# Kernel optimization log

Hardware: AMD Instinct MI355X
Metric: run time of the kernel (lower is better)

## Reference

```python
import jax, jax.numpy as jnp
import numpy as np

N = 20000      # nodes
E = 320000     # directed edges (before self loops)
IN_DIM = 384
D = 256        # hidden_dim
H = 4          # heads
C = D // H     # per-head channels = 64
L = 3          # layers
NEG_SLOPE = 0.2
LN_EPS = 1e-5


def setup_inputs() -> dict:
    key = jax.random.key(0)
    ks = jax.random.split(key, 8)
    return {
        "x": jax.random.normal(ks[0], (N, IN_DIM), jnp.float32),
        "edge_index": jax.random.randint(ks[1], (2, E), 0, N),
        "w_in": jax.random.normal(ks[2], (IN_DIM, D), jnp.float32) * 0.05,
        "b_in": jnp.zeros((D,), jnp.float32),
        "wl": jax.random.normal(ks[3], (L, D, D), jnp.float32) * 0.05,
        "wr": jax.random.normal(ks[4], (L, D, D), jnp.float32) * 0.05,
        "att": jax.random.normal(ks[5], (L, H, C), jnp.float32) * 0.05,
        "bias": jnp.zeros((L, D), jnp.float32),
        "ln_g": jnp.ones((L, D), jnp.float32),
        "ln_b": jnp.zeros((L, D), jnp.float32),
    }


def _layernorm(h, g, b):
    mu = jnp.mean(h, axis=-1, keepdims=True)
    var = jnp.mean(jnp.square(h - mu), axis=-1, keepdims=True)
    return (h - mu) * jax.lax.rsqrt(var + LN_EPS) * g + b


def _gatv2(h, src, dst, Wl, Wr, a, b):
    # PyG GATv2Conv, concat=True, eval mode (no dropout), self-loops already in src/dst.
    xl = (h @ Wl).reshape(N, H, C)   # source transform (lin_l)
    xr = (h @ Wr).reshape(N, H, C)   # target transform (lin_r)
    x_j = xl[src]                    # [E', H, C] gathered source messages
    e = jnp.einsum('ehc,hc->eh', jax.nn.leaky_relu(x_j + xr[dst], NEG_SLOPE), a)
    # segment softmax over edges grouped by destination node
    m = jax.ops.segment_max(e, dst, num_segments=N)
    e = jnp.exp(e - m[dst])
    s = jax.ops.segment_sum(e, dst, num_segments=N)
    alpha = e / (s[dst] + 1e-16)     # [E', H]
    out = jax.ops.segment_sum(x_j * alpha[:, :, None], dst, num_segments=N)
    return out.reshape(N, D) + b


def reference(x, edge_index, w_in, b_in, wl, wr, att, bias, ln_g, ln_b):
    loops = jnp.arange(N, dtype=edge_index.dtype)
    src = jnp.concatenate([edge_index[0], loops])
    dst = jnp.concatenate([edge_index[1], loops])
    h = x @ w_in + b_in
    for l in range(L):
        h_new = _layernorm(_gatv2(h, src, dst, wl[l], wr[l], att[l], bias[l]),
                           ln_g[l], ln_b[l])
        h = h + h_new  # shapes always match since concat output == hidden_dim
    norm = jnp.linalg.norm(h, axis=-1, keepdims=True)
    return h / jnp.maximum(norm, 1e-12)
```

## Files before the change

### kernel.cpp

```cpp
#include <hip/hip_runtime.h>
#include <math.h>

#define N_NODES 20000
#define E_EDGES 320000
#define E_TOT   (E_EDGES + N_NODES)
#define IN_DIM  384
#define DIM     256
#define LAYERS  3
#define NEG_SLOPE 0.2f
#define LN_EPS 1e-5f

typedef unsigned short u16;
typedef unsigned int u32;
typedef __attribute__((ext_vector_type(8))) short short8;
typedef __attribute__((ext_vector_type(8))) __bf16 bf16x8;
typedef __attribute__((ext_vector_type(4))) float f32x4;

__device__ inline u16 f2bf(float f) {
    u32 u = __builtin_bit_cast(u32, f);
    return (u16)((u + 0x7fffu + ((u >> 16) & 1u)) >> 16);
}
__device__ inline float bf2f(u16 s) {
    u32 u = (u32)s << 16;
    return __builtin_bit_cast(float, u);
}

__device__ inline float2 f2add(float2 a, float2 b) { return make_float2(a.x + b.x, a.y + b.y); }
__device__ inline float2 f2mul(float2 a, float2 b) { return make_float2(a.x * b.x, a.y * b.y); }
__device__ inline float2 f2fma(float2 a, float2 b, float2 c) {
    return make_float2(fmaf(a.x, b.x, c.x), fmaf(a.y, b.y, c.y));
}
__device__ inline float2 f2max(float2 a, float2 b) {
    return make_float2(fmaxf(a.x, b.x), fmaxf(a.y, b.y));
}

__device__ inline f32x4 mfma_bf16(short8 a, short8 b, f32x4 c) {
    return __builtin_amdgcn_mfma_f32_16x16x32_bf16(
        __builtin_bit_cast(bf16x8, a), __builtin_bit_cast(bf16x8, b), c, 0, 0, 0);
}

__device__ inline void gl_lds16(const u16* g, u16* l) {
    __builtin_amdgcn_global_load_lds(
        (const __attribute__((address_space(1))) u32*)g,
        (__attribute__((address_space(3))) u32*)l, 16, 0, 0);
}

#define W_IN_ELEMS (IN_DIM * DIM)
#define W_LR_ELEMS (2 * DIM * DIM)
#define W_TOT (W_IN_ELEMS + LAYERS * W_LR_ELEMS)

#define N4X (N_NODES * IN_DIM / 4)
__global__ void prep_kernel(const int* __restrict__ ei, int* __restrict__ counts,
                            const float* __restrict__ x, u16* __restrict__ x_bf,
                            const float* __restrict__ w_in, const float* __restrict__ wl,
                            const float* __restrict__ wr, u16* __restrict__ w_out) {
    int tid = blockIdx.x * 256 + threadIdx.x;
    if (tid < E_TOT) {
        int d = (tid < E_EDGES) ? ei[E_EDGES + tid] : (tid - E_EDGES);
        atomicAdd(&counts[d], 1);
        return;
    }
    tid -= E_TOT;
    if (tid < N4X) {
        float4 v = reinterpret_cast<const float4*>(x)[tid];
        reinterpret_cast<ushort4*>(x_bf)[tid] =
            make_ushort4(f2bf(v.x), f2bf(v.y), f2bf(v.z), f2bf(v.w));
        return;
    }
    tid -= N4X;
    if (tid < W_TOT) {
        float v;
        if (tid < W_IN_ELEMS) {
            int n = tid / IN_DIM, k = tid % IN_DIM;
            v = w_in[k * DIM + n];
        } else {
            int j = tid - W_IN_ELEMS;
            int l = j / W_LR_ELEMS;
            int r = j % W_LR_ELEMS;
            int n = r >> 8, k = r & 255;
            const float* W = (n < DIM) ? wl : wr;
            v = W[l * DIM * DIM + k * DIM + (n & 255)];
        }
        w_out[tid] = f2bf(v);
    }
}

__global__ __launch_bounds__(1024) void scan_kernel(const int* __restrict__ counts,
                                                    int* __restrict__ row_ptr) {
    __shared__ int sums[1024];
    const int t = threadIdx.x;
    const int CH = (N_NODES + 1023) / 1024;
    int base = t * CH;
    int local = 0;
    for (int i = 0; i < CH; ++i) {
        int idx = base + i;
        if (idx < N_NODES) local += counts[idx];
    }
    sums[t] = local;
    __syncthreads();
    for (int off = 1; off < 1024; off <<= 1) {
        int v = (t >= off) ? sums[t - off] : 0;
        __syncthreads();
        sums[t] += v;
        __syncthreads();
    }
    int run = (t == 0) ? 0 : sums[t - 1];
    for (int i = 0; i < CH; ++i) {
        int idx = base + i;
        if (idx < N_NODES) { row_ptr[idx] = run; run += counts[idx]; }
    }
    if (t == 1023) row_ptr[N_NODES] = sums[1023];
}

__global__ void scatter_kernel(const int* __restrict__ ei, const int* __restrict__ row_ptr,
                               int* __restrict__ cursor, int* __restrict__ csr_src) {
    int e = blockIdx.x * 256 + threadIdx.x;
    if (e >= E_TOT) return;
    int s, d;
    if (e < E_EDGES) { s = ei[e]; d = ei[E_EDGES + e]; }
    else { s = e - E_EDGES; d = s; }
    int pos = row_ptr[d] + atomicAdd(&cursor[d], 1);
    csr_src[pos] = s;
}

#define BM 128
#define BN 128
#define BK 64
template <int K, bool BIAS, int NX, int NTOT>
__global__ __launch_bounds__(256) void gemm_mfma(
    const u16* __restrict__ A, const u16* __restrict__ B,
    const float* __restrict__ bias, u16* __restrict__ Cbf,
    int M, int ldc) {
    __shared__ u16 lds[2][2][BM * BK];
    const int tid = threadIdx.x;
    const int w = tid >> 6, lane = tid & 63;
    const int wm = w >> 1, wn = w & 1;

    int lin = blockIdx.y * NX + blockIdx.x;
    constexpr int q8 = NTOT >> 3, r8 = NTOT & 7;
    int k8 = lin & 7, j8 = lin >> 3;
    int bid2 = k8 * q8 + min(k8, r8) + j8;
    const int bm = (bid2 / NX) * BM, bn = (bid2 % NX) * BN;

    const int fr = lane & 15, q = lane >> 4;

    f32x4 acc[4][4] = {};

    const int s_row = tid >> 3, s_blk = tid & 7;
    constexpr int NT = K / BK;

#pragma unroll
    for (int i = 0; i < 4; ++i) {
        int row = i * 32 + s_row;
        int gcol = ((s_blk ^ (row & 7)) << 3);
        int base = (i * 256 + (tid & ~63)) << 3;
        int ra = min(bm + row, M - 1);
        gl_lds16(A + (size_t)ra * K + gcol, &lds[0][0][base]);
        gl_lds16(B + (size_t)(bn + row) * K + gcol, &lds[0][1][base]);
    }
    __syncthreads();

    for (int t = 0; t < NT; ++t) {
        const int p = t & 1;
        if (t + 1 < NT) {
            const int k0 = (t + 1) * BK;
#pragma unroll
            for (int i = 0; i < 4; ++i) {
                int row = i * 32 + s_row;
                int gcol = ((s_blk ^ (row & 7)) << 3);
                int base = (i * 256 + (tid & ~63)) << 3;
                int ra = min(bm + row, M - 1);
                gl_lds16(A + (size_t)ra * K + k0 + gcol, &lds[p ^ 1][0][base]);
                gl_lds16(B + (size_t)(bn + row) * K + k0 + gcol, &lds[p ^ 1][1][base]);
            }
        }
        short8 a_f[2][4], b_f[2][4];
#pragma unroll
        for (int kk = 0; kk < 2; ++kk) {
#pragma unroll
            for (int mi = 0; mi < 4; ++mi) {
                int row = wm * 64 + mi * 16 + fr;
                a_f[kk][mi] = *reinterpret_cast<const short8*>(
                    &lds[p][0][row * BK + ((((kk << 2) + q) ^ (row & 7)) << 3)]);
            }
#pragma unroll
            for (int ni = 0; ni < 4; ++ni) {
                int row = wn * 64 + ni * 16 + fr;
                b_f[kk][ni] = *reinterpret_cast<const short8*>(
                    &lds[p][1][row * BK + ((((kk << 2) + q) ^ (row & 7)) << 3)]);
            }
        }
#pragma unroll
        for (int kk = 0; kk < 2; ++kk)
#pragma unroll
            for (int mi = 0; mi < 4; ++mi)
#pragma unroll
                for (int ni = 0; ni < 4; ++ni)
                    acc[mi][ni] = mfma_bf16(a_f[kk][mi], b_f[kk][ni], acc[mi][ni]);
        __syncthreads();
    }

#pragma unroll
    for (int mi = 0; mi < 4; ++mi) {
#pragma unroll
        for (int r = 0; r < 4; ++r) {
            int row = bm + wm * 64 + mi * 16 + q * 4 + r;
            if (row >= M) continue;
#pragma unroll
            for (int ni = 0; ni < 4; ++ni) {
                int col = bn + wn * 64 + ni * 16 + fr;
                float v = acc[mi][ni][r];
                if (BIAS) v += bias[col];
                Cbf[(size_t)row * ldc + col] = f2bf(v);
            }
        }
    }
}

template <bool LAST>
__global__ __launch_bounds__(256) void gat_edge(const u16* __restrict__ xlr_bf,
                                                const int* __restrict__ row_ptr,
                                                const int* __restrict__ csr_src,
                                                const float* __restrict__ att,
                                                const float* __restrict__ bias,
                                                const float* __restrict__ ln_g,
                                                const float* __restrict__ ln_b,
                                                u16* __restrict__ h_bf,
                                                float* __restrict__ out) {
    const int wave = threadIdx.x >> 6;
    const int lane = threadIdx.x & 63;
    const int node = blockIdx.x * 4 + wave;
    if (node >= N_NODES) return;
    const int c4 = lane << 2;

    const float4 a4 = *reinterpret_cast<const float4*>(att + c4);
    const float2 a01 = make_float2(a4.x, a4.y), a23 = make_float2(a4.z, a4.w);
    const ushort4 uxr = *reinterpret_cast<const ushort4*>(xlr_bf + (size_t)node * 512 + 256 + c4);
    const float2 xr01 = make_float2(bf2f(uxr.x), bf2f(uxr.y));
    const float2 xr23 = make_float2(bf2f(uxr.z), bf2f(uxr.w));
    const float2 k02 = make_float2(NEG_SLOPE, NEG_SLOPE);

    float sA = 0.f, sB = 0.f;
    float2 aA01 = make_float2(0.f, 0.f), aA23 = aA01, aB01 = aA01, aB23 = aA01;

    const int e0 = row_ptr[node];
    const int d = row_ptr[node + 1] - e0;

    for (int base = 0; base < d; base += 64) {
        const int rem = min(d - base, 64);
        const int idx = base + lane;
        const int my_src = (idx < d) ? csr_src[e0 + idx] : node;
        for (int k = 0; k < rem; k += 4) {
            ushort4 uu[4];
#pragma unroll
            for (int j = 0; j < 4; ++j) {
                int s = __shfl(my_src, k + j);
                uu[j] = *reinterpret_cast<const ushort4*>(xlr_bf + (size_t)s * 512 + c4);
            }
#pragma unroll
            for (int j = 0; j < 4; ++j) {
                float2 v01 = make_float2(bf2f(uu[j].x), bf2f(uu[j].y));
                float2 v23 = make_float2(bf2f(uu[j].z), bf2f(uu[j].w));
                float2 t01 = f2add(v01, xr01), t23 = f2add(v23, xr23);
                float2 l01 = f2max(t01, f2mul(t01, k02));
                float2 l23 = f2max(t23, f2mul(t23, k02));
                float2 dd = f2fma(l01, a01, f2mul(l23, a23));
                float p = dd.x + dd.y;
                p += __shfl_xor(p, 1);
                p += __shfl_xor(p, 2);
                p += __shfl_xor(p, 4);
                p += __shfl_xor(p, 8);
                float pe = (k + j < rem) ? __expf(p) : 0.f;
                float2 pe2 = make_float2(pe, pe);
                if (j & 1) {
                    sB += pe;
                    aB01 = f2fma(pe2, v01, aB01);
                    aB23 = f2fma(pe2, v23, aB23);
                } else {
                    sA += pe;
                    aA01 = f2fma(pe2, v01, aA01);
                    aA23 = f2fma(pe2, v23, aA23);
                }
            }
        }
    }

    float s = sA + sB;
    float inv = 1.f / (s + 1e-16f);
    float2 inv2 = make_float2(inv, inv);
    float2 acc01 = f2add(aA01, aB01), acc23 = f2add(aA23, aB23);
    const float4 b4 = *reinterpret_cast<const float4*>(bias + c4);
    float2 o01 = f2fma(acc01, inv2, make_float2(b4.x, b4.y));
    float2 o23 = f2fma(acc23, inv2, make_float2(b4.z, b4.w));

    float lsum = o01.x + o01.y + o23.x + o23.y;
    float lsq = o01.x * o01.x + o01.y * o01.y + o23.x * o23.x + o23.y * o23.y;
#pragma unroll
    for (int off = 1; off < 64; off <<= 1) {
        lsum += __shfl_xor(lsum, off);
        lsq  += __shfl_xor(lsq, off);
    }
    float mu = lsum * (1.f / 256.f);
    float var = lsq * (1.f / 256.f) - mu * mu;
    float rstd = rsqrtf(var + LN_EPS);
    const float4 g4  = *reinterpret_cast<const float4*>(ln_g + c4);
    const float4 lb4 = *reinterpret_cast<const float4*>(ln_b + c4);
    float2 mu2 = make_float2(-mu, -mu), rstd2 = make_float2(rstd, rstd);

    const ushort4 uh = *reinterpret_cast<const ushort4*>(h_bf + (size_t)node * DIM + c4);
    float2 h01 = make_float2(bf2f(uh.x), bf2f(uh.y));
    float2 h23 = make_float2(bf2f(uh.z), bf2f(uh.w));
    float2 n01 = f2fma(f2mul(f2add(o01, mu2), rstd2), make_float2(g4.x, g4.y),
                       make_float2(lb4.x, lb4.y));
    float2 n23 = f2fma(f2mul(f2add(o23, mu2), rstd2), make_float2(g4.z, g4.w),
                       make_float2(lb4.z, lb4.w));
    h01 = f2add(h01, n01);
    h23 = f2add(h23, n23);

    if (LAST) {
        float nsq = h01.x * h01.x + h01.y * h01.y + h23.x * h23.x + h23.y * h23.y;
#pragma unroll
        for (int off = 1; off < 64; off <<= 1) nsq += __shfl_xor(nsq, off);
        float ninv = 1.f / fmaxf(sqrtf(nsq), 1e-12f);
        float4 o = make_float4(h01.x * ninv, h01.y * ninv, h23.x * ninv, h23.y * ninv);
        *reinterpret_cast<float4*>(out + (size_t)node * DIM + c4) = o;
    } else {
        *reinterpret_cast<ushort4*>(h_bf + (size_t)node * DIM + c4) =
            make_ushort4(f2bf(h01.x), f2bf(h01.y), f2bf(h23.x), f2bf(h23.y));
    }
}

extern "C" void kernel_launch(void* const* d_in, const int* in_sizes, int n_in,
                              void* d_out, int out_size, void* d_ws, size_t ws_size,
                              hipStream_t stream) {
    const float* x    = (const float*)d_in[0];
    const int*   ei   = (const int*)d_in[1];
    const float* w_in = (const float*)d_in[2];
    const float* b_in = (const float*)d_in[3];
    const float* wl   = (const float*)d_in[4];
    const float* wr   = (const float*)d_in[5];
    const float* att  = (const float*)d_in[6];
    const float* bias = (const float*)d_in[7];
    const float* ln_g = (const float*)d_in[8];
    const float* ln_b = (const float*)d_in[9];

    char* p = (char*)d_ws;
    u16*   h_bf   = (u16*)p;              p += (size_t)N_NODES * DIM * 2;
    u16*   xlr_bf = (u16*)p;              p += (size_t)N_NODES * 512 * 2;
    u16*   w_bf   = (u16*)p;              p += (size_t)W_TOT * 2;
    int* row_ptr  = (int*)p;              p += (N_NODES + 1) * 4;
    int* counts   = (int*)p;              p += N_NODES * 4;
    int* cursor   = (int*)p;              p += N_NODES * 4;
    int* csr_src  = (int*)p;

    u16* x_bf = xlr_bf;

    hipMemsetAsync(counts, 0, sizeof(int) * 2 * N_NODES, stream);
    {
        int total = E_TOT + N4X + W_TOT;
        prep_kernel<<<(total + 255) / 256, 256, 0, stream>>>(
            ei, counts, x, x_bf, w_in, wl, wr, w_bf);
    }
    scan_kernel<<<1, 1024, 0, stream>>>(counts, row_ptr);
    scatter_kernel<<<(E_TOT + 255) / 256, 256, 0, stream>>>(ei, row_ptr, cursor, csr_src);

    constexpr int NYT = (N_NODES + BM - 1) / BM;
    gemm_mfma<IN_DIM, true, 2, 2 * NYT><<<dim3(2, NYT), 256, 0, stream>>>(
        x_bf, w_bf, b_in, h_bf, N_NODES, DIM);

    for (int l = 0; l < LAYERS; ++l) {
        const u16* wlr = w_bf + W_IN_ELEMS + (size_t)l * W_LR_ELEMS;
        gemm_mfma<DIM, false, 4, 4 * NYT><<<dim3(4, NYT), 256, 0, stream>>>(
            h_bf, wlr, nullptr, xlr_bf, N_NODES, 512);
        if (l < LAYERS - 1) {
            gat_edge<false><<<(N_NODES + 3) / 4, 256, 0, stream>>>(
                xlr_bf, row_ptr, csr_src,
                att + (size_t)l * DIM, bias + (size_t)l * DIM,
                ln_g + (size_t)l * DIM, ln_b + (size_t)l * DIM,
                h_bf, nullptr);
        } else {
            gat_edge<true><<<(N_NODES + 3) / 4, 256, 0, stream>>>(
                xlr_bf, row_ptr, csr_src,
                att + (size_t)l * DIM, bias + (size_t)l * DIM,
                ln_g + (size_t)l * DIM, ln_b + (size_t)l * DIM,
                h_bf, (float*)d_out);
        }
    }
}
```

Before: 260.1 us.

## Split each node's edges across two waves and use DPP reductions

The GAT edge kernel now assigns two waves to each destination node. Each wave processes half of the incoming edges, and the partial softmax sums and accumulators are combined through shared memory with a block barrier. Each wave reads source indices with scalar-style per-edge loads instead of shuffle broadcasts, and the 16-lane head reductions use DPP row operations in place of shfl_xor. The goal is more memory-level parallelism and shorter per-wave latency chains in the gather. In exchange the kernel launches twice as many waves, adds a __syncthreads, and the second wave of each pair sits idle during the LayerNorm epilogue.

```diff
diff --git a/kernel.cpp b/kernel.cpp
--- a/kernel.cpp
+++ b/kernel.cpp
@@ -32,6 +32,26 @@
 }
 __device__ inline float2 f2max(float2 a, float2 b) {
     return make_float2(fmaxf(a.x, b.x), fmaxf(a.y, b.y));
+}
+
+template <int CTRL>
+__device__ inline float dpp_add(float v) {
+    int x = __builtin_bit_cast(int, v);
+    int y = __builtin_amdgcn_update_dpp(0, x, CTRL, 0xF, 0xF, true);
+    return v + __builtin_bit_cast(float, y);
+}
+__device__ inline float red16(float p) {
+    p = dpp_add<0xB1>(p);
+    p = dpp_add<0x4E>(p);
+    p = dpp_add<0x141>(p);
+    p = dpp_add<0x140>(p);
+    return p;
+}
+__device__ inline float red64(float v) {
+    v = red16(v);
+    v += __shfl_xor(v, 16);
+    v += __shfl_xor(v, 32);
+    return v;
 }
 
 __device__ inline f32x4 mfma_bf16(short8 a, short8 b, f32x4 c) {
@@ -143,7 +163,6 @@
     const int bm = (bid2 / NX) * BM, bn = (bid2 % NX) * BN;
 
     const int fr = lane & 15, q = lane >> 4;
-
     f32x4 acc[4][4] = {};
 
     const int s_row = tid >> 3, s_blk = tid & 7;
@@ -227,10 +246,12 @@
                                                 const float* __restrict__ ln_b,
                                                 u16* __restrict__ h_bf,
                                                 float* __restrict__ out) {
+    __shared__ float comb[2][64][6];
     const int wave = threadIdx.x >> 6;
     const int lane = threadIdx.x & 63;
-    const int node = blockIdx.x * 4 + wave;
-    if (node >= N_NODES) return;
+    const int nsub = wave >> 1;
+    const int half = wave & 1;
+    const int node = blockIdx.x * 2 + nsub;
     const int c4 = lane << 2;
 
     const float4 a4 = *reinterpret_cast<const float4*>(att + c4);
@@ -240,66 +261,91 @@
     const float2 xr23 = make_float2(bf2f(uxr.z), bf2f(uxr.w));
     const float2 k02 = make_float2(NEG_SLOPE, NEG_SLOPE);
 
+    const int e0 = row_ptr[node];
+    const int d = row_ptr[node + 1] - e0;
+    const int dh = d >> 1;
+    const int me0 = e0 + (half ? dh : 0);
+    const int md  = half ? (d - dh) : dh;
+
     float sA = 0.f, sB = 0.f;
     float2 aA01 = make_float2(0.f, 0.f), aA23 = aA01, aB01 = aA01, aB23 = aA01;
 
-    const int e0 = row_ptr[node];
-    const int d = row_ptr[node + 1] - e0;
-
-    for (int base = 0; base < d; base += 64) {
-        const int rem = min(d - base, 64);
-        const int idx = base + lane;
-        const int my_src = (idx < d) ? csr_src[e0 + idx] : node;
-        for (int k = 0; k < rem; k += 4) {
-            ushort4 uu[4];
-#pragma unroll
-            for (int j = 0; j < 4; ++j) {
-                int s = __shfl(my_src, k + j);
-                uu[j] = *reinterpret_cast<const ushort4*>(xlr_bf + (size_t)s * 512 + c4);
-            }
-#pragma unroll
-            for (int j = 0; j < 4; ++j) {
-                float2 v01 = make_float2(bf2f(uu[j].x), bf2f(uu[j].y));
-                float2 v23 = make_float2(bf2f(uu[j].z), bf2f(uu[j].w));
-                float2 t01 = f2add(v01, xr01), t23 = f2add(v23, xr23);
-                float2 l01 = f2max(t01, f2mul(t01, k02));
-                float2 l23 = f2max(t23, f2mul(t23, k02));
-                float2 dd = f2fma(l01, a01, f2mul(l23, a23));
-                float p = dd.x + dd.y;
-                p += __shfl_xor(p, 1);
-                p += __shfl_xor(p, 2);
-                p += __shfl_xor(p, 4);
-                p += __shfl_xor(p, 8);
-                float pe = (k + j < rem) ? __expf(p) : 0.f;
-                float2 pe2 = make_float2(pe, pe);
-                if (j & 1) {
-                    sB += pe;
-                    aB01 = f2fma(pe2, v01, aB01);
-                    aB23 = f2fma(pe2, v23, aB23);
-                } else {
-                    sA += pe;
-                    aA01 = f2fma(pe2, v01, aA01);
-                    aA23 = f2fma(pe2, v23, aA23);
-                }
-            }
-        }
+    int e = 0;
+    for (; e + 1 < md; e += 2) {
+        int srcA = csr_src[me0 + e], srcB = csr_src[me0 + e + 1];
+        ushort4 ua = *reinterpret_cast<const ushort4*>(xlr_bf + (size_t)srcA * 512 + c4);
+        ushort4 ub = *reinterpret_cast<const ushort4*>(xlr_bf + (size_t)srcB * 512 + c4);
+
+        float2 va01 = make_float2(bf2f(ua.x), bf2f(ua.y));
+        float2 va23 = make_float2(bf2f(ua.z), bf2f(ua.w));
+        float2 vb01 = make_float2(bf2f(ub.x), bf2f(ub.y));
+        float2 vb23 = make_float2(bf2f(ub.z), bf2f(ub.w));
+
+        float2 ta01 = f2add(va01, xr01), ta23 = f2add(va23, xr23);
+        float2 la01 = f2max(ta01, f2mul(ta01, k02));
+        float2 la23 = f2max(ta23, f2mul(ta23, k02));
+        float2 dda = f2fma(la01, a01, f2mul(la23, a23));
+        float pA = red16(dda.x + dda.y);
+
+        float2 tb01 = f2add(vb01, xr01), tb23 = f2add(vb23, xr23);
+        float2 lb01 = f2max(tb01, f2mul(tb01, k02));
+        float2 lb23 = f2max(tb23, f2mul(tb23, k02));
+        float2 ddb = f2fma(lb01, a01, f2mul(lb23, a23));
+        float pB = red16(ddb.x + ddb.y);
+
+        float peA = __expf(pA);
+        float peB = __expf(pB);
+        sA += peA; sB += peB;
+        float2 peA2 = make_float2(peA, peA), peB2 = make_float2(peB, peB);
+        aA01 = f2fma(peA2, va01, aA01);
+        aA23 = f2fma(peA2, va23, aA23);
+        aB01 = f2fma(peB2, vb01, aB01);
+        aB23 = f2fma(peB2, vb23, aB23);
+    }
+    if (e < md) {
+        int srcA = csr_src[me0 + e];
+        ushort4 ua = *reinterpret_cast<const ushort4*>(xlr_bf + (size_t)srcA * 512 + c4);
+        float2 va01 = make_float2(bf2f(ua.x), bf2f(ua.y));
+        float2 va23 = make_float2(bf2f(ua.z), bf2f(ua.w));
+        float2 ta01 = f2add(va01, xr01), ta23 = f2add(va23, xr23);
+        float2 la01 = f2max(ta01, f2mul(ta01, k02));
+        float2 la23 = f2max(ta23, f2mul(ta23, k02));
+        float2 dda = f2fma(la01, a01, f2mul(la23, a23));
+        float pA = red16(dda.x + dda.y);
+        float peA = __expf(pA);
+        sA += peA;
+        float2 peA2 = make_float2(peA, peA);
+        aA01 = f2fma(peA2, va01, aA01);
+        aA23 = f2fma(peA2, va23, aA23);
     }
 
     float s = sA + sB;
+    float2 acc01 = f2add(aA01, aB01), acc23 = f2add(aA23, aB23);
+
+    if (half) {
+        comb[nsub][lane][0] = s;
+        comb[nsub][lane][1] = acc01.x;
+        comb[nsub][lane][2] = acc01.y;
+        comb[nsub][lane][3] = acc23.x;
+        comb[nsub][lane][4] = acc23.y;
+    }
+    __syncthreads();
+    if (half) return;
+
+    s += comb[nsub][lane][0];
+    acc01.x += comb[nsub][lane][1];
+    acc01.y += comb[nsub][lane][2];
+    acc23.x += comb[nsub][lane][3];
+    acc23.y += comb[nsub][lane][4];
+
     float inv = 1.f / (s + 1e-16f);
     float2 inv2 = make_float2(inv, inv);
-    float2 acc01 = f2add(aA01, aB01), acc23 = f2add(aA23, aB23);
     const float4 b4 = *reinterpret_cast<const float4*>(bias + c4);
     float2 o01 = f2fma(acc01, inv2, make_float2(b4.x, b4.y));
     float2 o23 = f2fma(acc23, inv2, make_float2(b4.z, b4.w));
 
-    float lsum = o01.x + o01.y + o23.x + o23.y;
-    float lsq = o01.x * o01.x + o01.y * o01.y + o23.x * o23.x + o23.y * o23.y;
-#pragma unroll
-    for (int off = 1; off < 64; off <<= 1) {
-        lsum += __shfl_xor(lsum, off);
-        lsq  += __shfl_xor(lsq, off);
-    }
+    float lsum = red64(o01.x + o01.y + o23.x + o23.y);
+    float lsq  = red64(o01.x * o01.x + o01.y * o01.y + o23.x * o23.x + o23.y * o23.y);
     float mu = lsum * (1.f / 256.f);
     float var = lsq * (1.f / 256.f) - mu * mu;
     float rstd = rsqrtf(var + LN_EPS);
@@ -318,9 +364,7 @@
     h23 = f2add(h23, n23);
 
     if (LAST) {
-        float nsq = h01.x * h01.x + h01.y * h01.y + h23.x * h23.x + h23.y * h23.y;
-#pragma unroll
-        for (int off = 1; off < 64; off <<= 1) nsq += __shfl_xor(nsq, off);
+        float nsq = red64(h01.x * h01.x + h01.y * h01.y + h23.x * h23.x + h23.y * h23.y);
         float ninv = 1.f / fmaxf(sqrtf(nsq), 1e-12f);
         float4 o = make_float4(h01.x * ninv, h01.y * ninv, h23.x * ninv, h23.y * ninv);
         *reinterpret_cast<float4*>(out + (size_t)node * DIM + c4) = o;
@@ -373,13 +417,13 @@
         gemm_mfma<DIM, false, 4, 4 * NYT><<<dim3(4, NYT), 256, 0, stream>>>(
             h_bf, wlr, nullptr, xlr_bf, N_NODES, 512);
         if (l < LAYERS - 1) {
-            gat_edge<false><<<(N_NODES + 3) / 4, 256, 0, stream>>>(
+            gat_edge<false><<<N_NODES / 2, 256, 0, stream>>>(
                 xlr_bf, row_ptr, csr_src,
                 att + (size_t)l * DIM, bias + (size_t)l * DIM,
                 ln_g + (size_t)l * DIM, ln_b + (size_t)l * DIM,
                 h_bf, nullptr);
         } else {
-            gat_edge<true><<<(N_NODES + 3) / 4, 256, 0, stream>>>(
+            gat_edge<true><<<N_NODES / 2, 256, 0, stream>>>(
                 xlr_bf, row_ptr, csr_src,
                 att + (size_t)l * DIM, bias + (size_t)l * DIM,
                 ln_g + (size_t)l * DIM, ln_b + (size_t)l * DIM,
```

Measured after the change: 250.2 us. 3.8% less time.
